# Performance work log

Hardware: AMD Instinct MI355X
Metric: run time of the kernel (lower is better)

## Reference

```python
import jax, jax.numpy as jnp
import numpy as np

T, H, NH, HD, I = 2048, 2048, 16, 128, 8192
EPS = 1e-6


def rotate_every_two(x):
    # result[..., 2i] = -x[..., 2i+1]; result[..., 2i+1] = x[..., 2i]
    x1 = x[..., ::2]
    x2 = x[..., 1::2]
    return jnp.stack((-x2, x1), axis=-1).reshape(x.shape)


def setup_inputs() -> dict:
    key = jax.random.key(0)
    ks = jax.random.split(key, 10)
    x = jax.random.normal(ks[0], (T, H), dtype=jnp.float32)
    normed_ages = jax.random.normal(ks[1], (T,), dtype=jnp.float32)
    sin = jax.random.uniform(ks[2], (T, 1, HD), dtype=jnp.float32)
    cos = jax.random.uniform(ks[3], (T, 1, HD), dtype=jnp.float32)
    attn_bias = jax.random.normal(ks[4], (1, NH, T, T), dtype=jnp.float32) * 0.02
    norm_w = jnp.ones((H,), dtype=jnp.float32)
    w_in = jax.random.normal(ks[5], (H, 3 * H + 2 * I), dtype=jnp.float32) / np.sqrt(H)
    b_in = jnp.zeros((3 * H + 2 * I,), dtype=jnp.float32)
    w_out = jax.random.normal(ks[6], (H + I, H), dtype=jnp.float32) / np.sqrt(H + I)
    b_out = jnp.zeros((H,), dtype=jnp.float32)
    return {"x": x, "normed_ages": normed_ages, "sin": sin, "cos": cos,
            "attn_bias": attn_bias, "norm_w": norm_w, "w_in": w_in,
            "b_in": b_in, "w_out": w_out, "b_out": b_out}


def reference(x, normed_ages, sin, cos, attn_bias, norm_w, b_in, b_out, w_in, w_out):
    # RMSNorm
    xn = x * jax.lax.rsqrt(jnp.mean(x * x, axis=-1, keepdims=True) + EPS) * norm_w
    # use_normed_ages: overwrite last two feature columns
    xn = xn.at[:, -2].set(normed_ages)
    xn = xn.at[:, -1].set(normed_ages * normed_ages)
    # fused input projection: [T, 2I (ff) | 3H (qkv)]
    t = xn @ w_in + b_in
    ff = t[:, : 2 * I]
    qkv = t[:, 2 * I:].reshape(T, 3, NH, HD)
    q = qkv[:, 0] * cos + rotate_every_two(qkv[:, 0]) * sin  # [T, NH, HD]
    k = qkv[:, 1] * cos + rotate_every_two(qkv[:, 1]) * sin
    v = qkv[:, 2]
    # attention (xformers memory_efficient_attention semantics, scale 1/sqrt(HD))
    scores = jnp.einsum('thd,shd->hts', q, k) / np.sqrt(HD) + attn_bias[0]
    probs = jax.nn.softmax(scores, axis=-1)
    attn = jnp.einsum('hts,shd->thd', probs, v).reshape(T, H)
    # SwiGLU
    x1, x2 = ff[:, :I], ff[:, I:]
    ff = jax.nn.silu(x1) * x2
    combined = jnp.concatenate((attn, ff), axis=-1)  # [T, H+I]
    return combined @ w_out + b_out
```

## Files before the change

kernel.cpp:

```cpp
#include <hip/hip_runtime.h>
#include <stdint.h>

typedef unsigned short u16;
typedef __attribute__((ext_vector_type(8))) short short8;
typedef __attribute__((ext_vector_type(4))) short short4v;
typedef __attribute__((ext_vector_type(4))) float floatx4;

#define T_DIM 2048
#define NH    16
#define HD    128
#define H_DIM 2048
#define I_DIM 8192
#define NCOL1 22528
#define NCOL2 10240
#define PADW  1036
#define KSPLIT 4
#define KSLEN  (NCOL2 / KSPLIT)

__device__ __forceinline__ float bf2f(u16 b) {
  union { uint32_t u; float f; } x; x.u = ((uint32_t)b) << 16; return x.f;
}
__device__ __forceinline__ u16 f2bf(float f) {
  union { float f; uint32_t u; } x; x.f = f;
  uint32_t r = x.u + 0x7fffu + ((x.u >> 16) & 1u);
  return (u16)(r >> 16);
}

__device__ __forceinline__ void gl_lds16(const void* g, void* l) {
  __builtin_amdgcn_global_load_lds((const __attribute__((address_space(1))) void*)g,
                                   (__attribute__((address_space(3))) void*)l, 16, 0, 0);
}

__device__ __forceinline__ floatx4 mfma32(short8 a, short8 b, floatx4 c) {
  return __builtin_amdgcn_mfma_f32_16x16x32_bf16(a, b, c, 0, 0, 0);
}
__device__ __forceinline__ floatx4 mfma16(short4v a, short4v b, floatx4 c) {
#if __has_builtin(__builtin_amdgcn_mfma_f32_16x16x16bf16_1k)
  return __builtin_amdgcn_mfma_f32_16x16x16bf16_1k(a, b, c, 0, 0, 0);
#else
  asm volatile("v_mfma_f32_16x16x16_bf16 %0, %1, %2, %0" : "+v"(c) : "v"(a), "v"(b));
  return c;
#endif
}

__global__ __launch_bounds__(256) void rmsnorm_k(
    const float* __restrict__ x, const float* __restrict__ ages,
    const float* __restrict__ w, u16* __restrict__ xn) {
  int t = blockIdx.x, tid = threadIdx.x;
  const float* xr = x + (size_t)t * H_DIM;
  floatx4 a = *(const floatx4*)(xr + tid * 8);
  floatx4 b = *(const floatx4*)(xr + tid * 8 + 4);
  float ss = a[0]*a[0]+a[1]*a[1]+a[2]*a[2]+a[3]*a[3]
           + b[0]*b[0]+b[1]*b[1]+b[2]*b[2]+b[3]*b[3];
#pragma unroll
  for (int off = 32; off >= 1; off >>= 1) ss += __shfl_xor(ss, off);
  __shared__ float red[4];
  if ((tid & 63) == 0) red[tid >> 6] = ss;
  __syncthreads();
  float tot = red[0] + red[1] + red[2] + red[3];
  float rms = rsqrtf(tot * (1.0f / H_DIM) + 1e-6f);
  const float* wr = w + tid * 8;
  float v[8] = {a[0],a[1],a[2],a[3],b[0],b[1],b[2],b[3]};
  short8 o;
#pragma unroll
  for (int i = 0; i < 8; ++i) o[i] = (short)f2bf(v[i] * rms * wr[i]);
  if (tid == 255) {
    float ag = ages[t];
    o[6] = (short)f2bf(ag);
    o[7] = (short)f2bf(ag * ag);
  }
  *(short8*)(xn + (size_t)t * H_DIM + tid * 8) = o;
}

__global__ __launch_bounds__(256) void transpose_f32_bf16(
    const float* __restrict__ in, u16* __restrict__ out, int K, int N) {
  __shared__ float tile[32][33];
  int n0 = blockIdx.x * 32, k0 = blockIdx.y * 32;
  int c = threadIdx.x & 31, r = threadIdx.x >> 5;
#pragma unroll
  for (int i = 0; i < 4; ++i) {
    int kk = r + i * 8;
    tile[c][kk] = in[(size_t)(k0 + kk) * N + n0 + c];
  }
  __syncthreads();
#pragma unroll
  for (int i = 0; i < 4; ++i) {
    int nn = r + i * 8;
    out[(size_t)(n0 + nn) * K + k0 + c] = f2bf(tile[nn][c]);
  }
}

template<int OUTF>
__global__ __launch_bounds__(512, 2) void gemm256(
    const u16* __restrict__ A, const u16* __restrict__ B,
    const float* __restrict__ bias, void* __restrict__ Cout,
    int M, int N, int K, int klen) {
  __shared__ __align__(16) u16 sm[65536];
  int nbm = M >> 8, nbn = N >> 8;
  int per = nbm * nbn;
  int nwg = per * (K / klen);
  int bid = blockIdx.x;
  int swz = (bid & 7) * (nwg >> 3) + (bid >> 3);
  int sp = swz / per, rr = swz % per;
  int bn = rr / nbm, bm = rr % nbm;
  int kbeg = sp * klen;
  int tid = threadIdx.x, lane = tid & 63;
  int wid = tid >> 6;
  int wrow = wid >> 2;
  int wcol = wid & 3;
  int lq = lane & 15, lg = lane >> 4;

  int srow = tid >> 2;
  int scol = ((tid & 3) ^ ((tid >> 3) & 3)) << 3;
  const u16* Ag0 = A + (size_t)(bm * 256 + srow) * K + kbeg + scol;
  const u16* Ag1 = Ag0 + (size_t)128 * K;
  const u16* Bg0 = B + (size_t)(bn * 256 + srow) * K + kbeg + scol;
  const u16* Bg1 = Bg0 + (size_t)128 * K;
  u16* Ad0 = sm + tid * 8;
  u16* Ad1 = sm + 4096 + tid * 8;
  u16* Bd0 = sm + 8192 + tid * 8;
  u16* Bd1 = sm + 12288 + tid * 8;

  int xorc = ((lq >> 1) & 3) << 3;
  int aoff = (wrow * 128 + lq) * 32 + ((lg * 8) ^ xorc);
  int boff = 8192 + (wcol * 64 + lq) * 32 + ((lg * 8) ^ xorc);

  floatx4 acc[8][4] = {};
  const int NT = klen >> 5;

  auto STAGE = [&](int t) {
    int sl = (t & 3) * 16384;
    int ko = t * 32;
    gl_lds16(Ag0 + ko, Ad0 + sl);
    gl_lds16(Ag1 + ko, Ad1 + sl);
    gl_lds16(Bg0 + ko, Bd0 + sl);
    gl_lds16(Bg1 + ko, Bd1 + sl);
  };

  STAGE(0); STAGE(1); STAGE(2);
  asm volatile("s_waitcnt vmcnt(8)\n\ts_barrier" ::: "memory");

  for (int t = 0; t < NT; ++t) {
    if (t + 3 < NT) STAGE(t + 3);
    const u16* sb = sm + (t & 3) * 16384;
    short8 af[8], bfr[4];
#pragma unroll
    for (int i = 0; i < 8; ++i) af[i]  = *(const short8*)(sb + aoff + i * 512);
#pragma unroll
    for (int i = 0; i < 4; ++i) bfr[i] = *(const short8*)(sb + boff + i * 512);
    __builtin_amdgcn_s_setprio(1);
#pragma unroll
    for (int mi = 0; mi < 8; ++mi)
#pragma unroll
      for (int ni = 0; ni < 4; ++ni)
        acc[mi][ni] = mfma32(af[mi], bfr[ni], acc[mi][ni]);
    __builtin_amdgcn_s_setprio(0);
    if (t + 3 < NT) asm volatile("s_waitcnt vmcnt(8)\n\ts_barrier" ::: "memory");
    else            asm volatile("s_waitcnt vmcnt(0)\n\ts_barrier" ::: "memory");
  }

#pragma unroll
  for (int mi = 0; mi < 8; ++mi) {
#pragma unroll
    for (int ni = 0; ni < 4; ++ni) {
      int col = bn * 256 + wcol * 64 + ni * 16 + lq;
      float bv = (OUTF == 2) ? 0.f : bias[col];
#pragma unroll
      for (int j = 0; j < 4; ++j) {
        int row = bm * 256 + wrow * 128 + mi * 16 + lg * 4 + j;
        float vv = acc[mi][ni][j] + bv;
        if (OUTF == 0)      ((u16*)Cout)[(size_t)row * N + col] = f2bf(vv);
        else if (OUTF == 1) ((float*)Cout)[(size_t)row * N + col] = vv;
        else ((float*)Cout)[(size_t)sp * M * N + (size_t)row * N + col] = vv;
      }
    }
  }
}

__global__ __launch_bounds__(256) void reduce_split(
    const float* __restrict__ part, const float* __restrict__ bias,
    float* __restrict__ out) {
  size_t idx = ((size_t)blockIdx.x * 256 + threadIdx.x) * 4;
  int col = (int)(idx & (H_DIM - 1));
  floatx4 acc = *(const floatx4*)(bias + col);
#pragma unroll
  for (int s = 0; s < KSPLIT; ++s) {
    floatx4 p = *(const floatx4*)(part + (size_t)s * T_DIM * H_DIM + idx);
#pragma unroll
    for (int j = 0; j < 4; ++j) acc[j] += p[j];
  }
  *(floatx4*)(out + idx) = acc;
}

__global__ __launch_bounds__(256) void rope_split(
    const u16* __restrict__ tb, const float* __restrict__ sinp, const float* __restrict__ cosp,
    u16* __restrict__ qb, u16* __restrict__ kf, u16* __restrict__ vf) {
  __shared__ u16 vtile[32][130];
  int t0 = blockIdx.x * 32, h = blockIdx.y, tid = threadIdx.x;
  int r = tid >> 3, d0 = (tid & 7) << 4;
  int t = t0 + r;
  const u16* base = tb + (size_t)t * NCOL1 + 2 * I_DIM + h * HD + d0;
  const float* cp = cosp + (size_t)t * HD + d0;
  const float* sp = sinp + (size_t)t * HD + d0;
  float cv[16], sv[16];
#pragma unroll
  for (int i = 0; i < 16; i += 4) {
    *(floatx4*)(cv + i) = *(const floatx4*)(cp + i);
    *(floatx4*)(sv + i) = *(const floatx4*)(sp + i);
  }
#pragma unroll
  for (int s = 0; s < 2; ++s) {
    const u16* src = base + s * (NH * HD);
    short8 x0 = *(const short8*)src;
    short8 x1 = *(const short8*)(src + 8);
    float xf[16];
#pragma unroll
    for (int i = 0; i < 8; ++i) { xf[i] = bf2f((u16)x0[i]); xf[8 + i] = bf2f((u16)x1[i]); }
    short8 o0, o1;
#pragma unroll
    for (int i = 0; i < 8; i += 2) {
      o0[i]     = (short)f2bf(xf[i] * cv[i] - xf[i + 1] * sv[i]);
      o0[i + 1] = (short)f2bf(xf[i + 1] * cv[i + 1] + xf[i] * sv[i + 1]);
      o1[i]     = (short)f2bf(xf[8 + i] * cv[8 + i] - xf[9 + i] * sv[8 + i]);
      o1[i + 1] = (short)f2bf(xf[9 + i] * cv[9 + i] + xf[8 + i] * sv[9 + i]);
    }
    if (s == 0) {
      u16* dst = qb + ((size_t)h * T_DIM + t) * HD + d0;
      *(short8*)dst = o0;
      *(short8*)(dst + 8) = o1;
    } else {
      int s16 = t >> 4, tt = d0 >> 5, lg0 = (d0 >> 3) & 3;
      size_t cb = (((size_t)h * 128 + s16) * 4 + tt) * 512 + ((t & 15) + 16 * lg0) * 8;
      *(short8*)(kf + cb) = o0;
      *(short8*)(kf + cb + 128) = o1;
    }
  }
  short8 v0 = *(const short8*)(base + 2 * NH * HD);
  short8 v1 = *(const short8*)(base + 2 * NH * HD + 8);
#pragma unroll
  for (int i = 0; i < 8; ++i) {
    vtile[r][d0 + i]     = (u16)v0[i];
    vtile[r][d0 + 8 + i] = (u16)v1[i];
  }
  __syncthreads();
  {
    int d = tid >> 1, th = (tid & 1) << 4;
    int s16 = (t0 + th) >> 4;
    int dp = d >> 5, par = (d >> 4) & 1, lqv = d & 15;
    size_t cb = (((size_t)h * 128 + s16) * 4 + dp) * 512 + par * 4;
#pragma unroll
    for (int lg = 0; lg < 4; ++lg) {
      short4v g;
#pragma unroll
      for (int j = 0; j < 4; ++j) g[j] = (short)vtile[th + lg * 4 + j][d];
      *(short4v*)(vf + cb + (size_t)(lqv + 16 * lg) * 8) = g;
    }
  }
}

__global__ __launch_bounds__(256) void silu_mul(
    const u16* __restrict__ tb, u16* __restrict__ comb) {
  int idx = blockIdx.x * 256 + threadIdx.x;
  int t = idx >> 10;
  int j = (idx & 1023) << 3;
  const u16* p1 = tb + (size_t)t * NCOL1 + j;
  const u16* p2 = p1 + I_DIM;
  short8 a = *(const short8*)p1;
  short8 b = *(const short8*)p2;
  short8 o;
#pragma unroll
  for (int i = 0; i < 8; ++i) {
    float x1 = bf2f((u16)a[i]), x2 = bf2f((u16)b[i]);
    float s = x1 / (1.0f + __expf(-x1));
    o[i] = (short)f2bf(s * x2);
  }
  *(short8*)(comb + (size_t)t * NCOL2 + H_DIM + j) = o;
}

__global__ __launch_bounds__(256) void attn_fused(
    const u16* __restrict__ Q, const u16* __restrict__ kf,
    const u16* __restrict__ vf, const float* __restrict__ bias,
    u16* __restrict__ comb) {
  __shared__ float lds[16 * PADW];
  int bid = blockIdx.x;
  int swz = (bid & 7) * 256 + (bid >> 3);
  int h = swz >> 7, qt = swz & 127;
  int q0 = qt * 16;
  int tid = threadIdx.x;
  int w = tid >> 6, lane = tid & 63;
  int lq = lane & 15, lg = lane >> 4;

  const u16* Qp = Q + ((size_t)h * T_DIM + q0 + lq) * HD + lg * 8;
  const u16* Kf = kf + ((size_t)h * 128) * 2048 + lane * 8;
  const u16* Vf = vf + ((size_t)h * 128) * 2048 + lane * 8;
  const float* Bh = bias + ((size_t)h * T_DIM + q0) * T_DIM;

  short8 qf[4];
#pragma unroll
  for (int t = 0; t < 4; ++t) qf[t] = *(const short8*)(Qp + t * 32);

  floatx4 o[8] = {};
  float m = -1e30f, l = 0.f;
  const float sc = 0.08838834764831845f;

#pragma unroll
  for (int tile = 0; tile < 2; ++tile) {
#pragma unroll
    for (int r = 0; r < 16; ++r) {
      const float* src = Bh + (size_t)r * T_DIM + tile * 1024 + tid * 4;
      gl_lds16(src, &lds[r * PADW + tid * 4]);
    }
    __syncthreads();
#pragma unroll
    for (int sub = 0; sub < 8; ++sub) {
      int soff = sub * 128 + w * 32;
      int s0 = tile * 1024 + soff;
      int s16a = s0 >> 4;
      const u16* ka = Kf + (size_t)s16a * 2048;
      floatx4 st0 = {0.f,0.f,0.f,0.f}, st1 = {0.f,0.f,0.f,0.f};
#pragma unroll
      for (int t = 0; t < 4; ++t) {
        st0 = mfma32(*(const short8*)(ka + t * 512), qf[t], st0);
        st1 = mfma32(*(const short8*)(ka + 2048 + t * 512), qf[t], st1);
      }
      floatx4 b0 = *(const floatx4*)&lds[lq * PADW + soff + lg * 4];
      floatx4 b1 = *(const floatx4*)&lds[lq * PADW + soff + lg * 4 + 16];
      float p[8]; float tmax = -1e30f;
#pragma unroll
      for (int j = 0; j < 4; ++j) {
        p[j]     = st0[j] * sc + b0[j];
        p[4 + j] = st1[j] * sc + b1[j];
        tmax = fmaxf(tmax, fmaxf(p[j], p[4 + j]));
      }
      tmax = fmaxf(tmax, __shfl_xor(tmax, 16));
      tmax = fmaxf(tmax, __shfl_xor(tmax, 32));
      float mn = fmaxf(m, tmax);
      float alpha = __expf(m - mn);
      float rs = 0.f;
      short4v pb0, pb1;
#pragma unroll
      for (int j = 0; j < 4; ++j) {
        float e0 = __expf(p[j] - mn), e1 = __expf(p[4 + j] - mn);
        rs += e0 + e1;
        pb0[j] = (short)f2bf(e0);
        pb1[j] = (short)f2bf(e1);
      }
      rs += __shfl_xor(rs, 16);
      rs += __shfl_xor(rs, 32);
      l = l * alpha + rs; m = mn;
#pragma unroll
      for (int dt = 0; dt < 8; ++dt) o[dt] *= alpha;
      const u16* vb = Vf + (size_t)s16a * 2048;
#pragma unroll
      for (int dp = 0; dp < 4; ++dp) {
        short8 wa = *(const short8*)(vb + dp * 512);
        short8 wb = *(const short8*)(vb + 2048 + dp * 512);
        short4v a0 = {wa[0], wa[1], wa[2], wa[3]};
        short4v a1 = {wa[4], wa[5], wa[6], wa[7]};
        short4v c0 = {wb[0], wb[1], wb[2], wb[3]};
        short4v c1 = {wb[4], wb[5], wb[6], wb[7]};
        o[2*dp]     = mfma16(a0, pb0, o[2*dp]);
        o[2*dp + 1] = mfma16(a1, pb0, o[2*dp + 1]);
        o[2*dp]     = mfma16(c0, pb1, o[2*dp]);
        o[2*dp + 1] = mfma16(c1, pb1, o[2*dp + 1]);
      }
    }
    __syncthreads();
  }

  if (lg == 0) { lds[8448 + w * 16 + lq] = m; lds[8512 + w * 16 + lq] = l; }
  __syncthreads();
  float M = -1e30f;
#pragma unroll
  for (int i = 0; i < 4; ++i) M = fmaxf(M, lds[8448 + i * 16 + lq]);
  float scale = __expf(m - M);
#pragma unroll
  for (int dt = 0; dt < 8; ++dt) {
    floatx4 so = o[dt] * scale;
    *(floatx4*)&lds[w * 2112 + lq * 132 + dt * 16 + lg * 4] = so;
  }
  __syncthreads();
  {
    int row = tid >> 4, d0 = (tid & 15) * 8;
    float M2 = -1e30f;
#pragma unroll
    for (int i = 0; i < 4; ++i) M2 = fmaxf(M2, lds[8448 + i * 16 + row]);
    float den = 0.f;
#pragma unroll
    for (int i = 0; i < 4; ++i)
      den += __expf(lds[8448 + i * 16 + row] - M2) * lds[8512 + i * 16 + row];
    float inv = 1.0f / den;
    short8 ov;
#pragma unroll
    for (int k = 0; k < 8; ++k) {
      float s = 0.f;
#pragma unroll
      for (int i = 0; i < 4; ++i) s += lds[i * 2112 + row * 132 + d0 + k];
      ov[k] = (short)f2bf(s * inv);
    }
    *(short8*)(comb + (size_t)(q0 + row) * NCOL2 + h * HD + d0) = ov;
  }
}

extern "C" void kernel_launch(void* const* d_in, const int* in_sizes, int n_in,
                              void* d_out, int out_size, void* d_ws, size_t ws_size,
                              hipStream_t stream) {
  (void)in_sizes; (void)n_in; (void)out_size; (void)ws_size;
  const float* x     = (const float*)d_in[0];
  const float* ages  = (const float*)d_in[1];
  const float* sinp  = (const float*)d_in[2];
  const float* cosp  = (const float*)d_in[3];
  const float* bias  = (const float*)d_in[4];
  const float* normw = (const float*)d_in[5];
  const float* w_in  = (const float*)d_in[6];
  const float* b_in  = (const float*)d_in[7];
  const float* w_out = (const float*)d_in[8];
  const float* b_out = (const float*)d_in[9];

  char* ws = (char*)d_ws;
  const size_t SZ_XN   = (size_t)T_DIM * H_DIM * 2;
  const size_t SZ_W1T  = (size_t)NCOL1 * H_DIM * 2;
  const size_t SZ_T    = (size_t)T_DIM * NCOL1 * 2;
  const size_t SZ_HEAD = (size_t)NH * T_DIM * HD * 2;
  u16* xn   = (u16*)(ws);
  u16* w1t  = (u16*)(ws + SZ_XN);
  u16* tb   = (u16*)(ws + SZ_XN + SZ_W1T);
  u16* qb   = (u16*)(ws + SZ_XN + SZ_W1T + SZ_T);
  u16* kf   = (u16*)(ws + SZ_XN + SZ_W1T + SZ_T + SZ_HEAD);
  u16* vf   = (u16*)(ws + SZ_XN + SZ_W1T + SZ_T + 2 * SZ_HEAD);
  u16* w2t  = (u16*)(ws + SZ_XN);
  u16* comb = (u16*)(ws + SZ_XN + (48ull << 20));
  float* part = (float*)tb;

  rmsnorm_k<<<T_DIM, 256, 0, stream>>>(x, ages, normw, xn);
  transpose_f32_bf16<<<dim3(NCOL1 / 32, H_DIM / 32), 256, 0, stream>>>(w_in, w1t, H_DIM, NCOL1);
  gemm256<0><<<(T_DIM / 256) * (NCOL1 / 256), 512, 0, stream>>>(
      xn, w1t, b_in, tb, T_DIM, NCOL1, H_DIM, H_DIM);
  rope_split<<<dim3(T_DIM / 32, NH), 256, 0, stream>>>(tb, sinp, cosp, qb, kf, vf);
  silu_mul<<<(T_DIM * I_DIM) / (256 * 8), 256, 0, stream>>>(tb, comb);
  transpose_f32_bf16<<<dim3(H_DIM / 32, NCOL2 / 32), 256, 0, stream>>>(w_out, w2t, NCOL2, H_DIM);
  attn_fused<<<NH * (T_DIM / 16), 256, 0, stream>>>(qb, kf, vf, bias, comb);
  gemm256<2><<<(T_DIM / 256) * (H_DIM / 256) * KSPLIT, 512, 0, stream>>>(
      comb, w2t, b_out, part, T_DIM, H_DIM, NCOL2, KSLEN);
  reduce_split<<<(T_DIM * H_DIM / 4) / 256, 256, 0, stream>>>(part, b_out, (float*)d_out);
}
```

Baseline: 548.3 us.

## Split GEMM k-step into two MFMA halves with interleaved prefetch; use 128-row tiles for output GEMM

Templates the GEMM on the number of 128-row A halves, so the output projection uses 128x256 tiles and launches twice as many workgroups. Each k-step is split into two MFMA phases, with the A and B prefetches issued between LDS fragment reads and separated by extra barriers. The intent is to overlap global-to-LDS traffic with MFMA work and to improve occupancy and wave balance for the smaller GEMM. The cost is more barriers per iteration and lower data reuse per tile in the second GEMM.

New measurement: 580.3 us. +5.8%, slower.

```diff
diff --git a/kernel.cpp b/kernel.cpp
--- a/kernel.cpp
+++ b/kernel.cpp
@@ -17,6 +17,9 @@
 #define KSPLIT 4
 #define KSLEN  (NCOL2 / KSPLIT)
 
+#define VMBAR(n) asm volatile("s_waitcnt vmcnt(" #n ")\n\ts_barrier" ::: "memory")
+#define SBAR()   asm volatile("s_barrier" ::: "memory")
+
 __device__ __forceinline__ float bf2f(u16 b) {
   union { uint32_t u; float f; } x; x.u = ((uint32_t)b) << 16; return x.f;
 }
@@ -90,13 +93,16 @@
   }
 }
 
-template<int OUTF>
+template<int OUTF, int NAH>
 __global__ __launch_bounds__(512, 2) void gemm256(
     const u16* __restrict__ A, const u16* __restrict__ B,
     const float* __restrict__ bias, void* __restrict__ Cout,
     int M, int N, int K, int klen) {
-  __shared__ __align__(16) u16 sm[65536];
-  int nbm = M >> 8, nbn = N >> 8;
+  constexpr int BM   = NAH * 128;
+  constexpr int SLOT = (NAH + 2) * 4096;
+  constexpr int MI   = NAH * 4;
+  __shared__ __align__(16) u16 sm[4 * SLOT];
+  int nbm = M / BM, nbn = N >> 8;
   int per = nbm * nbn;
   int nwg = per * (K / klen);
   int bid = blockIdx.x;
@@ -112,62 +118,84 @@
 
   int srow = tid >> 2;
   int scol = ((tid & 3) ^ ((tid >> 3) & 3)) << 3;
-  const u16* Ag0 = A + (size_t)(bm * 256 + srow) * K + kbeg + scol;
-  const u16* Ag1 = Ag0 + (size_t)128 * K;
-  const u16* Bg0 = B + (size_t)(bn * 256 + srow) * K + kbeg + scol;
-  const u16* Bg1 = Bg0 + (size_t)128 * K;
-  u16* Ad0 = sm + tid * 8;
-  u16* Ad1 = sm + 4096 + tid * 8;
-  u16* Bd0 = sm + 8192 + tid * 8;
-  u16* Bd1 = sm + 12288 + tid * 8;
+  const u16* Ag[NAH]; u16* Ad[NAH];
+  const u16* Bg[2];   u16* Bd[2];
+#pragma unroll
+  for (int i = 0; i < NAH; ++i) {
+    Ag[i] = A + (size_t)(bm * BM + i * 128 + srow) * K + kbeg + scol;
+    Ad[i] = sm + i * 4096 + tid * 8;
+  }
+#pragma unroll
+  for (int i = 0; i < 2; ++i) {
+    Bg[i] = B + (size_t)(bn * 256 + i * 128 + srow) * K + kbeg + scol;
+    Bd[i] = sm + NAH * 4096 + i * 4096 + tid * 8;
+  }
 
   int xorc = ((lq >> 1) & 3) << 3;
-  int aoff = (wrow * 128 + lq) * 32 + ((lg * 8) ^ xorc);
-  int boff = 8192 + (wcol * 64 + lq) * 32 + ((lg * 8) ^ xorc);
-
-  floatx4 acc[8][4] = {};
+  int aoff = (wrow * (64 * NAH) + lq) * 32 + ((lg * 8) ^ xorc);
+  int boff = NAH * 4096 + (wcol * 64 + lq) * 32 + ((lg * 8) ^ xorc);
+
+  floatx4 acc[MI][4] = {};
   const int NT = klen >> 5;
 
-  auto STAGE = [&](int t) {
-    int sl = (t & 3) * 16384;
-    int ko = t * 32;
-    gl_lds16(Ag0 + ko, Ad0 + sl);
-    gl_lds16(Ag1 + ko, Ad1 + sl);
-    gl_lds16(Bg0 + ko, Bd0 + sl);
-    gl_lds16(Bg1 + ko, Bd1 + sl);
+  auto STAGE_A = [&](int t) {
+    int sl = (t & 3) * SLOT, ko = t * 32;
+#pragma unroll
+    for (int i = 0; i < NAH; ++i) gl_lds16(Ag[i] + ko, Ad[i] + sl);
   };
-
-  STAGE(0); STAGE(1); STAGE(2);
-  asm volatile("s_waitcnt vmcnt(8)\n\ts_barrier" ::: "memory");
+  auto STAGE_B = [&](int t) {
+    int sl = (t & 3) * SLOT, ko = t * 32;
+#pragma unroll
+    for (int i = 0; i < 2; ++i) gl_lds16(Bg[i] + ko, Bd[i] + sl);
+  };
+
+  STAGE_A(0); STAGE_B(0); STAGE_A(1); STAGE_B(1); STAGE_A(2); STAGE_B(2);
+  if constexpr (NAH == 2) VMBAR(8); else VMBAR(6);
 
   for (int t = 0; t < NT; ++t) {
-    if (t + 3 < NT) STAGE(t + 3);
-    const u16* sb = sm + (t & 3) * 16384;
-    short8 af[8], bfr[4];
-#pragma unroll
-    for (int i = 0; i < 8; ++i) af[i]  = *(const short8*)(sb + aoff + i * 512);
+    const u16* sb = sm + (t & 3) * SLOT;
+    bool pf = (t + 3 < NT);
+    short8 af0[2 * NAH], bfr[4];
+#pragma unroll
+    for (int i = 0; i < 2 * NAH; ++i) af0[i] = *(const short8*)(sb + aoff + i * 512);
 #pragma unroll
     for (int i = 0; i < 4; ++i) bfr[i] = *(const short8*)(sb + boff + i * 512);
+    if (pf) STAGE_A(t + 3);
+    SBAR();
     __builtin_amdgcn_s_setprio(1);
 #pragma unroll
-    for (int mi = 0; mi < 8; ++mi)
+    for (int mi = 0; mi < 2 * NAH; ++mi)
 #pragma unroll
       for (int ni = 0; ni < 4; ++ni)
-        acc[mi][ni] = mfma32(af[mi], bfr[ni], acc[mi][ni]);
+        acc[mi][ni] = mfma32(af0[mi], bfr[ni], acc[mi][ni]);
     __builtin_amdgcn_s_setprio(0);
-    if (t + 3 < NT) asm volatile("s_waitcnt vmcnt(8)\n\ts_barrier" ::: "memory");
-    else            asm volatile("s_waitcnt vmcnt(0)\n\ts_barrier" ::: "memory");
-  }
-
-#pragma unroll
-  for (int mi = 0; mi < 8; ++mi) {
+    SBAR();
+    short8 af1[2 * NAH];
+#pragma unroll
+    for (int i = 0; i < 2 * NAH; ++i)
+      af1[i] = *(const short8*)(sb + aoff + (2 * NAH + i) * 512);
+    if (pf) STAGE_B(t + 3);
+    SBAR();
+    __builtin_amdgcn_s_setprio(1);
+#pragma unroll
+    for (int mi = 0; mi < 2 * NAH; ++mi)
+#pragma unroll
+      for (int ni = 0; ni < 4; ++ni)
+        acc[2 * NAH + mi][ni] = mfma32(af1[mi], bfr[ni], acc[2 * NAH + mi][ni]);
+    __builtin_amdgcn_s_setprio(0);
+    if (pf) { if constexpr (NAH == 2) VMBAR(8); else VMBAR(6); }
+    else    VMBAR(0);
+  }
+
+#pragma unroll
+  for (int mi = 0; mi < MI; ++mi) {
 #pragma unroll
     for (int ni = 0; ni < 4; ++ni) {
       int col = bn * 256 + wcol * 64 + ni * 16 + lq;
       float bv = (OUTF == 2) ? 0.f : bias[col];
 #pragma unroll
       for (int j = 0; j < 4; ++j) {
-        int row = bm * 256 + wrow * 128 + mi * 16 + lg * 4 + j;
+        int row = bm * BM + wrow * (64 * NAH) + mi * 16 + lg * 4 + j;
         float vv = acc[mi][ni][j] + bv;
         if (OUTF == 0)      ((u16*)Cout)[(size_t)row * N + col] = f2bf(vv);
         else if (OUTF == 1) ((float*)Cout)[(size_t)row * N + col] = vv;
@@ -434,13 +462,13 @@
 
   rmsnorm_k<<<T_DIM, 256, 0, stream>>>(x, ages, normw, xn);
   transpose_f32_bf16<<<dim3(NCOL1 / 32, H_DIM / 32), 256, 0, stream>>>(w_in, w1t, H_DIM, NCOL1);
-  gemm256<0><<<(T_DIM / 256) * (NCOL1 / 256), 512, 0, stream>>>(
+  gemm256<0, 2><<<(T_DIM / 256) * (NCOL1 / 256), 512, 0, stream>>>(
       xn, w1t, b_in, tb, T_DIM, NCOL1, H_DIM, H_DIM);
   rope_split<<<dim3(T_DIM / 32, NH), 256, 0, stream>>>(tb, sinp, cosp, qb, kf, vf);
   silu_mul<<<(T_DIM * I_DIM) / (256 * 8), 256, 0, stream>>>(tb, comb);
   transpose_f32_bf16<<<dim3(H_DIM / 32, NCOL2 / 32), 256, 0, stream>>>(w_out, w2t, NCOL2, H_DIM);
   attn_fused<<<NH * (T_DIM / 16), 256, 0, stream>>>(qb, kf, vf, bias, comb);
-  gemm256<2><<<(T_DIM / 256) * (H_DIM / 256) * KSPLIT, 512, 0, stream>>>(
+  gemm256<2, 1><<<(T_DIM / 128) * (H_DIM / 256) * KSPLIT, 512, 0, stream>>>(
       comb, w2t, b_out, part, T_DIM, H_DIM, NCOL2, KSLEN);
   reduce_split<<<(T_DIM * H_DIM / 4) / 256, 256, 0, stream>>>(part, b_out, (float*)d_out);
 }
```

## Software-pipeline LDS fragment reads across two K-steps in the GEMM main loop

Applied to the files above, without the earlier changes.

Unrolls the GEMM K-loop by two and loads the next tile's A/B fragments from LDS into a second register set while the current tile's MFMAs run. Global-to-LDS staging waits change from vmcnt(8) to vmcnt(4), because two staged tiles must already be resident before the early reads. The aim is to hide LDS read latency behind matrix work. In exchange it uses more vector registers, which can cut occupancy, and it assumes an even number of K tiles.

After: 543.6 us, median of 2. About the same (-0.8%).

```diff
diff --git a/kernel.cpp b/kernel.cpp
--- a/kernel.cpp
+++ b/kernel.cpp
@@ -16,6 +16,8 @@
 #define PADW  1036
 #define KSPLIT 4
 #define KSLEN  (NCOL2 / KSPLIT)
+
+#define VMBAR(n) asm volatile("s_waitcnt vmcnt(" #n ")\n\ts_barrier" ::: "memory")
 
 __device__ __forceinline__ float bf2f(u16 b) {
   union { uint32_t u; float f; } x; x.u = ((uint32_t)b) << 16; return x.f;
@@ -137,26 +139,51 @@
     gl_lds16(Bg1 + ko, Bd1 + sl);
   };
 
+  short8 a47[4];
+  short8 aX[4], bX[4], aY[4], bY[4];
+
+  auto RD_A47 = [&](int slot) {
+    const u16* sb = sm + slot * 16384;
+#pragma unroll
+    for (int i = 0; i < 4; ++i) a47[i] = *(const short8*)(sb + aoff + (4 + i) * 512);
+  };
+  auto RD_PF = [&](int slot, short8* a, short8* b) {
+    const u16* sb = sm + slot * 16384;
+#pragma unroll
+    for (int i = 0; i < 4; ++i) a[i] = *(const short8*)(sb + aoff + i * 512);
+#pragma unroll
+    for (int i = 0; i < 4; ++i) b[i] = *(const short8*)(sb + boff + i * 512);
+  };
+  auto COMPUTE = [&](short8* a03, short8* b) {
+    __builtin_amdgcn_s_setprio(1);
+#pragma unroll
+    for (int mi = 0; mi < 4; ++mi)
+#pragma unroll
+      for (int ni = 0; ni < 4; ++ni)
+        acc[mi][ni] = mfma32(a03[mi], b[ni], acc[mi][ni]);
+#pragma unroll
+    for (int mi = 4; mi < 8; ++mi)
+#pragma unroll
+      for (int ni = 0; ni < 4; ++ni)
+        acc[mi][ni] = mfma32(a47[mi - 4], b[ni], acc[mi][ni]);
+    __builtin_amdgcn_s_setprio(0);
+  };
+
   STAGE(0); STAGE(1); STAGE(2);
-  asm volatile("s_waitcnt vmcnt(8)\n\ts_barrier" ::: "memory");
-
-  for (int t = 0; t < NT; ++t) {
+  VMBAR(4);
+  RD_PF(0, aX, bX);
+
+  for (int t = 0; t < NT; t += 2) {
+    RD_A47(t & 3);
+    RD_PF((t + 1) & 3, aY, bY);
     if (t + 3 < NT) STAGE(t + 3);
-    const u16* sb = sm + (t & 3) * 16384;
-    short8 af[8], bfr[4];
-#pragma unroll
-    for (int i = 0; i < 8; ++i) af[i]  = *(const short8*)(sb + aoff + i * 512);
-#pragma unroll
-    for (int i = 0; i < 4; ++i) bfr[i] = *(const short8*)(sb + boff + i * 512);
-    __builtin_amdgcn_s_setprio(1);
-#pragma unroll
-    for (int mi = 0; mi < 8; ++mi)
-#pragma unroll
-      for (int ni = 0; ni < 4; ++ni)
-        acc[mi][ni] = mfma32(af[mi], bfr[ni], acc[mi][ni]);
-    __builtin_amdgcn_s_setprio(0);
-    if (t + 3 < NT) asm volatile("s_waitcnt vmcnt(8)\n\ts_barrier" ::: "memory");
-    else            asm volatile("s_waitcnt vmcnt(0)\n\ts_barrier" ::: "memory");
+    COMPUTE(aX, bX);
+    if (t + 3 < NT) VMBAR(4); else VMBAR(0);
+    RD_A47((t + 1) & 3);
+    if (t + 2 < NT) RD_PF((t + 2) & 3, aX, bX);
+    if (t + 4 < NT) STAGE(t + 4);
+    COMPUTE(aY, bY);
+    if (t + 4 < NT) VMBAR(4); else VMBAR(0);
   }
 
 #pragma unroll
```
